# Kernel optimization log

Measured on AMD Instinct MI355X. Metric: run time of the kernel, lower is better.

## Reference

```python
import jax, jax.numpy as jnp
import numpy as np

# Straight-through sign binarization (Binarize in BNN code mutates .data, so
# autograd sees identity -> custom_vjp with identity backward).
@jax.custom_vjp
def binarize(x):
    return jnp.sign(x)

def _bin_fwd(x):
    return jnp.sign(x), None

def _bin_bwd(_, g):
    return (g,)

binarize.defvjp(_bin_fwd, _bin_bwd)

EPS = 1e-5  # torch BatchNorm1d default eps

def batchnorm(x, g, b):
    # training-mode BN: batch statistics, biased variance
    if x.ndim == 3:  # (N, C, L): stats over N and L
        m = x.mean(axis=(0, 2), keepdims=True)
        v = x.var(axis=(0, 2), keepdims=True)
        return (x - m) / jnp.sqrt(v + EPS) * g[None, :, None] + b[None, :, None]
    m = x.mean(axis=0)
    v = x.var(axis=0)
    return (x - m) / jnp.sqrt(v + EPS) * g + b

def hardtanh(x):
    return jnp.clip(x, -1.0, 1.0)

def maxpool3(x):
    # MaxPool1d(kernel=3, stride=3): trim then reshape-max
    N, C, L = x.shape
    Lp = L // 3
    return x[:, :, :Lp * 3].reshape(N, C, Lp, 3).max(axis=-1)

def bconv(x, w, b, binarize_input=True):
    # BinarizeConv1d: kernel 41, dilation 2, VALID padding; weights sign-binarized,
    # inputs binarized except when in_channels == 3 (first layer rule in BNN code).
    xb = binarize(x) if binarize_input else x
    wb = binarize(w)
    y = jax.lax.conv_general_dilated(
        xb, wb, window_strides=(1,), padding='VALID',
        rhs_dilation=(2,), dimension_numbers=('NCH', 'OIH', 'NCH'))
    return y + b[None, :, None]

def blinear(x, w, b):
    # BinarizeLinear: in_features 832/1024 != 784 -> binarize input and weight
    return binarize(x) @ binarize(w).T + b

def _forward(x, bn0_g, bn0_b, conv1_w, conv1_b, bn1_g, bn1_b,
             conv2_w, conv2_b, bn2_g, bn2_b, conv3_w, conv3_b,
             bn3_g, bn3_b, conv4_w, conv4_b, bn4_g, bn4_b,
             conv5_w, conv5_b, fc1_w, fc1_b, bn5_g, bn5_b,
             fc2_w, fc2_b, bn6_g, bn6_b):
    h = hardtanh(batchnorm(x, bn0_g, bn0_b))
    h = maxpool3(bconv(h, conv1_w, conv1_b, binarize_input=False))  # (N,64,5306)
    h = hardtanh(batchnorm(h, bn1_g, bn1_b))
    h = maxpool3(bconv(h, conv2_w, conv2_b))  # (N,64,1742)
    h = hardtanh(batchnorm(h, bn2_g, bn2_b))
    h = maxpool3(bconv(h, conv3_w, conv3_b))  # (N,64,554)
    h = hardtanh(batchnorm(h, bn3_g, bn3_b))
    h = maxpool3(bconv(h, conv4_w, conv4_b))  # (N,64,158)
    h = hardtanh(batchnorm(h, bn4_g, bn4_b))
    h = maxpool3(bconv(h, conv5_w, conv5_b))  # (N,32,26)
    h = h.reshape(-1, 16 * 52)                # (N, 832)
    h = hardtanh(batchnorm(blinear(h, fc1_w, fc1_b), bn5_g, bn5_b))
    h = batchnorm(blinear(h, fc2_w, fc2_b), bn6_g, bn6_b)
    return jax.nn.log_softmax(h, axis=1)

def setup_inputs() -> dict:
    key = jax.random.key(0)
    ks = jax.random.split(key, 32)
    def rn(k, shape, s=0.1):
        return jax.random.normal(k, shape, dtype=jnp.float32) * s
    def bn_params(kg, kb, c):
        return 1.0 + rn(kg, (c,)), rn(kb, (c,))
    N, L, K = 64, 16000, 41
    d = {"x": jax.random.normal(ks[0], (N, 3, L), dtype=jnp.float32)}
    d["bn0_g"], d["bn0_b"] = bn_params(ks[1], ks[2], 3)
    d["conv1_w"], d["conv1_b"] = rn(ks[3], (64, 3, K)), rn(ks[4], (64,), 0.01)
    d["bn1_g"], d["bn1_b"] = bn_params(ks[5], ks[6], 64)
    d["conv2_w"], d["conv2_b"] = rn(ks[7], (64, 64, K)), rn(ks[8], (64,), 0.01)
    d["bn2_g"], d["bn2_b"] = bn_params(ks[9], ks[10], 64)
    d["conv3_w"], d["conv3_b"] = rn(ks[11], (64, 64, K)), rn(ks[12], (64,), 0.01)
    d["bn3_g"], d["bn3_b"] = bn_params(ks[13], ks[14], 64)
    d["conv4_w"], d["conv4_b"] = rn(ks[15], (64, 64, K)), rn(ks[16], (64,), 0.01)
    d["bn4_g"], d["bn4_b"] = bn_params(ks[17], ks[18], 64)
    d["conv5_w"], d["conv5_b"] = rn(ks[19], (32, 64, K)), rn(ks[20], (32,), 0.01)
    d["fc1_w"], d["fc1_b"] = rn(ks[21], (1024, 832)), rn(ks[22], (1024,), 0.01)
    d["bn5_g"], d["bn5_b"] = bn_params(ks[23], ks[24], 1024)
    d["fc2_w"], d["fc2_b"] = rn(ks[25], (1000, 1024)), rn(ks[26], (1000,), 0.01)
    d["bn6_g"], d["bn6_b"] = bn_params(ks[27], ks[28], 1000)
    return d

def reference(x, bn0_g, bn0_b, conv1_w, conv1_b, bn1_g, bn1_b,
              conv2_w, conv2_b, bn2_g, bn2_b, conv3_w, conv3_b,
              bn3_g, bn3_b, conv4_w, conv4_b, bn4_g, bn4_b,
              conv5_w, conv5_b, fc1_w, fc1_b, bn5_g, bn5_b,
              fc2_w, fc2_b, bn6_g, bn6_b):
    return _forward(x, bn0_g, bn0_b, conv1_w, conv1_b, bn1_g, bn1_b,
                    conv2_w, conv2_b, bn2_g, bn2_b, conv3_w, conv3_b,
                    bn3_g, bn3_b, conv4_w, conv4_b, bn4_g, bn4_b,
                    conv5_w, conv5_b, fc1_w, fc1_b, bn5_g, bn5_b,
                    fc2_w, fc2_b, bn6_g, bn6_b)
```

## Files before the change

kernel.cpp:

```cpp
#include <hip/hip_runtime.h>
#include <hip/hip_bf16.h>
#include <stdint.h>

typedef __hip_bfloat16 bf16;
typedef unsigned long long u64;
typedef unsigned short u16;

typedef __attribute__((ext_vector_type(8))) short bf16x8;
typedef __attribute__((ext_vector_type(4))) float f32x4;

#define FIXCAP (1u << 20)

static __device__ __forceinline__ float ldin(const void* p, long i, int f32) {
    return f32 ? ((const float*)p)[i] : __bfloat162float(((const bf16*)p)[i]);
}

__global__ void k_probe(const void* x, unsigned* ctl) {
    int tid = threadIdx.x;
    int good = 0;
    for (int i = tid; i < 1024; i += 256) {
        float v = __bfloat162float(((const bf16*)x)[2 * i]);
        float a = fabsf(v);
        if (v == 0.0f || (isfinite(v) && a >= 1e-4f && a <= 100.0f)) good++;
    }
    __shared__ int s[256];
    s[tid] = good; __syncthreads();
    for (int st = 128; st > 0; st >>= 1) {
        if (tid < st) s[tid] += s[tid + st];
        __syncthreads();
    }
    if (tid == 0) { ctl[0] = 0u; ctl[1] = (s[0] >= 700) ? 0u : 1u; }
}

__global__ void k_sentinel(void* outv, const unsigned* ctl, float val) {
    int i = blockIdx.x * 256 + threadIdx.x;
    if (i >= 64000) return;
    if (ctl[1]) ((float*)outv)[i] = val;
    else ((bf16*)outv)[i] = __float2bfloat16(val);
}

__device__ __forceinline__ void pack_convw_task(const void* w, uint2* wp, int Co, int f32,
                                                int bx, int tid) {
    int t = bx * 256 + tid;
    if (t >= Co * 41) return;
    int co = t / 41, k = t % 41;
    unsigned w0 = 0, w1 = 0;
    for (int c = 0; c < 32; c++)
        if (ldin(w, (co * 64 + c) * 41 + k, f32) > 0.f) w0 |= (1u << c);
    for (int c = 0; c < 32; c++)
        if (ldin(w, (co * 64 + 32 + c) * 41 + k, f32) > 0.f) w1 |= (1u << c);
    wp[t] = make_uint2(w0, w1);
}
__device__ __forceinline__ void pack_rows_task(const void* w, unsigned* wp, int rows, int F,
                                               int f32, int bx, int tid) {
    int Fw = F >> 5;
    int t = bx * 256 + tid;
    if (t >= rows * Fw) return;
    int r = t / Fw, wi = t % Fw;
    unsigned m = 0;
    for (int j = 0; j < 32; j++)
        if (ldin(w, (long)r * F + wi * 32 + j, f32) > 0.f) m |= (1u << j);
    wp[t] = m;
}

__global__ void k_prep(const void* x, const void* c1w, const void* c2w, const void* c3w,
                       const void* c4w, const void* c5w, const void* f1w, const void* f2w,
                       u16* afrag, uint2* w2p, uint2* w3p, uint2* w4p, uint2* w5p,
                       unsigned* fc1wp, unsigned* fc2wp, u64* stats, double* part0,
                       const unsigned* ctl) {
    int f32 = ctl[1];
    int task = blockIdx.y, bx = blockIdx.x, tid = threadIdx.x;
    switch (task) {
        case 0: {
            int t = bx * 256 + tid;
            if (t < 2304) {
                int m = t / 576, rem = t - m * 576;
                int ks = rem / 64, lane = rem - ks * 64;
                int li = lane & 15, hq = lane >> 4;
                int row = 16 * m + li;
                int g = 4 * ks + hq;
                int c = g / 11, t0 = 4 * (g - 11 * c);
                u16* outp = afrag + (size_t)t * 8;
                for (int i2 = 0; i2 < 4; i2++) {
                    int tt = t0 + i2;
                    u16 sv = 0;
                    if (g < 33 && tt <= 40) {
                        float wv = ldin(c1w, (row * 3 + c) * 41 + tt, f32);
                        sv = (wv > 0.f) ? (u16)0x3F80 : ((wv < 0.f) ? (u16)0xBF80 : (u16)0);
                    }
                    outp[2 * i2] = sv;
                    outp[2 * i2 + 1] = sv;
                }
            }
        } break;
        case 1: pack_convw_task(c2w, w2p, 64, f32, bx, tid); break;
        case 2: pack_convw_task(c3w, w3p, 64, f32, bx, tid); break;
        case 3: pack_convw_task(c4w, w4p, 64, f32, bx, tid); break;
        case 4: pack_convw_task(c5w, w5p, 32, f32, bx, tid); break;
        case 5: pack_rows_task(f1w, fc1wp, 1024, 832, f32, bx, tid); break;
        case 6: pack_rows_task(f2w, fc2wp, 1000, 1024, f32, bx, tid); break;
        case 7: {
            int i = bx * 256 + tid;
            if (i < 14400) stats[i] = 0ull;
        } break;
        case 8: {
            if (bx >= 96) return;
            int c = bx >> 5, s = bx & 31;
            double s1 = 0, s2 = 0;
            for (int n = 0; n < 64; n++) {
                long base = (long)(n * 3 + c) * 16000;
                for (int l = s * 256 + tid; l < 16000; l += 32 * 256) {
                    double v = (double)ldin(x, base + l, f32);
                    s1 += v; s2 += v * v;
                }
            }
            __shared__ double a1[256], a2[256];
            a1[tid] = s1; a2[tid] = s2;
            __syncthreads();
            for (int st = 128; st > 0; st >>= 1) {
                if (tid < st) { a1[tid] += a1[tid + st]; a2[tid] += a2[tid + st]; }
                __syncthreads();
            }
            if (tid == 0) { part0[(c * 32 + s) * 2] = a1[0]; part0[(c * 32 + s) * 2 + 1] = a2[0]; }
        } break;
    }
}

__global__ __launch_bounds__(256, 4) void k_conv1(const void* __restrict__ x,
                                                  const double* __restrict__ part0,
                                                  const void* __restrict__ g0,
                                                  const void* __restrict__ b0,
                                                  const u16* __restrict__ afrag,
                                                  float* __restrict__ yq,
                                                  double* __restrict__ yb,
                                                  const unsigned* __restrict__ ctl) {
    __shared__ unsigned xs[8][140];
    __shared__ float pool[4][48][16];
    __shared__ double sbuf[4][64][2];
    __shared__ double2 b0s[3];
    int f32 = ctl[1];
    int n = blockIdx.y, bx = blockIdx.x, tid = threadIdx.x;
    if (tid < 3) {
        int c = tid;
        double s1 = 0, s2 = 0;
        for (int s = 0; s < 32; s++) { s1 += part0[(c * 32 + s) * 2]; s2 += part0[(c * 32 + s) * 2 + 1]; }
        double M = 64.0 * 16000.0;
        double mu = s1 / M, var = s2 / M - mu * mu;
        double A = (double)ldin(g0, c, f32) / sqrt(var + 1e-5);
        b0s[c] = make_double2(A, (double)ldin(b0, c, f32) - mu * A);
    }
    __syncthreads();

    unsigned* xsf = &xs[0][0];
    for (int f = tid; f < 1120; f += 256) {
        int rc = f / 140, qi = f - rc * 140;
        int r = rc >> 2, c = rc & 3;
        unsigned dw = 0u;
        if (c < 3) {
            int xpos = 192 * bx + 2 * qi + r;
            if (xpos < 16000) {
                double2 pb = b0s[c];
                double v = (double)ldin(x, (long)(n * 3 + c) * 16000 + xpos, f32) * pb.x + pb.y;
                v = fmin(fmax(v, -1.0), 1.0);
                float xf = (float)v;
                bf16 h = __float2bfloat16(xf);
                float hf = __bfloat162float(h);
                bf16 lo = __float2bfloat16(xf - hf);
                dw = (unsigned)__bfloat16_as_ushort(h) | ((unsigned)__bfloat16_as_ushort(lo) << 16);
            }
        }
        xsf[f] = dw;
    }
    __syncthreads();

    int lane = tid & 63;
    int li = lane & 15, hq = lane >> 4;
    int w = __builtin_amdgcn_readfirstlane(tid >> 6);

    f32x4 zz = {0.f, 0.f, 0.f, 0.f};
    f32x4 acc[4][3];
#pragma unroll
    for (int m = 0; m < 4; m++)
#pragma unroll
        for (int nf = 0; nf < 3; nf++) acc[m][nf] = zz;

    int boff[3];
#pragma unroll
    for (int nf = 0; nf < 3; nf++) {
        int pl = 48 * w + 16 * nf + li;
        boff[nf] = (pl & 1) * 560 + (pl >> 1);
    }

    const bf16x8* ag = (const bf16x8*)afrag;
#pragma unroll 1
    for (int ks = 0; ks < 9; ks++) {
        int g = 4 * ks + hq;
        int c = g / 11;
        int kb = c * 140 + 4 * (g - 11 * c);
        bf16x8 a0 = ag[(0 * 9 + ks) * 64 + lane];
        bf16x8 a1 = ag[(1 * 9 + ks) * 64 + lane];
        bf16x8 a2 = ag[(2 * 9 + ks) * 64 + lane];
        bf16x8 a3 = ag[(3 * 9 + ks) * 64 + lane];
#pragma unroll
        for (int nf = 0; nf < 3; nf++) {
            const unsigned* bp = xsf + boff[nf] + kb;
            union { int4 i4; bf16x8 v; } u;
            u.i4 = make_int4(bp[0], bp[1], bp[2], bp[3]);
            acc[0][nf] = __builtin_amdgcn_mfma_f32_16x16x32_bf16(a0, u.v, acc[0][nf], 0, 0, 0);
            acc[1][nf] = __builtin_amdgcn_mfma_f32_16x16x32_bf16(a1, u.v, acc[1][nf], 0, 0, 0);
            acc[2][nf] = __builtin_amdgcn_mfma_f32_16x16x32_bf16(a2, u.v, acc[2][nf], 0, 0, 0);
            acc[3][nf] = __builtin_amdgcn_mfma_f32_16x16x32_bf16(a3, u.v, acc[3][nf], 0, 0, 0);
        }
    }

    int lp0 = 64 * bx + 16 * w;
#pragma unroll 1
    for (int m = 0; m < 4; m++) {
#pragma unroll
        for (int nf = 0; nf < 3; nf++)
            *(f32x4*)&pool[w][16 * nf + li][4 * hq] = acc[m][nf];
        double s = 0.0, q = 0.0;
#pragma unroll
        for (int i = 0; i < 4; i++) {
            int pc = hq + 4 * i;
            float mq = fmaxf(fmaxf(pool[w][3 * pc][li], pool[w][3 * pc + 1][li]),
                             pool[w][3 * pc + 2][li]);
            int lp = lp0 + pc;
            if (lp < 5306) {
                yq[((size_t)n * 64 + 16 * m + li) * 5306 + lp] = mq;
                double d = (double)mq;
                s += d; q += d * d;
            }
        }
        s += __shfl_down(s, 32, 64); s += __shfl_down(s, 16, 64);
        q += __shfl_down(q, 32, 64); q += __shfl_down(q, 16, 64);
        if (lane < 16) { sbuf[w][16 * m + lane][0] = s; sbuf[w][16 * m + lane][1] = q; }
    }
    __syncthreads();
    if (tid < 64) {
        double s = sbuf[0][tid][0] + sbuf[1][tid][0] + sbuf[2][tid][0] + sbuf[3][tid][0];
        double q = sbuf[0][tid][1] + sbuf[1][tid][1] + sbuf[2][tid][1] + sbuf[3][tid][1];
        int sb = bx & 15;
        atomicAdd(&yb[(tid * 16 + sb) * 2], s);
        atomicAdd(&yb[(tid * 16 + sb) * 2 + 1], q);
    }
}

__global__ void k_pack_y(const float* __restrict__ yq, const double* __restrict__ yb,
                         const void* g1, const void* b1,
                         uint2* __restrict__ xp,
                         unsigned* __restrict__ fixcnt, unsigned* __restrict__ fixlist,
                         const unsigned* __restrict__ ctl) {
    __shared__ double2 pqs[64];
    int f32 = ctl[1];
    int tid = threadIdx.x;
    if (tid < 64) {
        int c = tid;
        double s1 = 0, s2 = 0;
        for (int s = 0; s < 16; s++) { s1 += yb[(c * 16 + s) * 2]; s2 += yb[(c * 16 + s) * 2 + 1]; }
        double M = 64.0 * 5306.0;
        double mu = s1 / M;
        double var = s2 / M - mu * mu;
        double A = (double)ldin(g1, c, f32) / sqrt(var + 1e-5);
        pqs[c] = make_double2(A, (double)ldin(b1, c, f32) - mu * A);
    }
    __syncthreads();
    int n = blockIdx.y;
    int l = blockIdx.x * 256 + tid;
    if (l >= 5306) return;
    unsigned w0 = 0, w1 = 0;
    for (int c = 0; c < 64; c++) {
        double2 p = pqs[c];
        double v = (double)yq[((size_t)n * 64 + c) * 5306 + l] * p.x + p.y;
        if (fabs(v) < 2e-3 * fabs(p.x)) {
            unsigned idx = atomicAdd(fixcnt, 1u);
            if (idx < FIXCAP) fixlist[idx] = ((unsigned)n << 19) | ((unsigned)c << 13) | (unsigned)l;
        }
        if (v > 0.0) { if (c < 32) w0 |= 1u << c; else w1 |= 1u << (c - 32); }
    }
    xp[(size_t)n * 5306 + l] = make_uint2(w0, w1);
}

__global__ void k_fix(const unsigned* __restrict__ fixcnt, const unsigned* __restrict__ fixlist,
                      const double* __restrict__ yb, const void* g1, const void* b1,
                      const void* __restrict__ x, const void* __restrict__ c1w,
                      const double* __restrict__ part0, const void* g0, const void* b0,
                      unsigned* __restrict__ x2p, const unsigned* __restrict__ ctl) {
    int f32 = ctl[1];
    unsigned cnt = min(*fixcnt, FIXCAP);
    for (unsigned t = blockIdx.x * 256 + threadIdx.x; t < cnt; t += gridDim.x * 256) {
        unsigned e = fixlist[t];
        int n = e >> 19, c = (e >> 13) & 63, l = e & 8191;
        double s1 = 0, s2 = 0;
        for (int s = 0; s < 16; s++) { s1 += yb[(c * 16 + s) * 2]; s2 += yb[(c * 16 + s) * 2 + 1]; }
        double M = 64.0 * 5306.0;
        double mu = s1 / M, var = s2 / M - mu * mu;
        double A = (double)ldin(g1, c, f32) / sqrt(var + 1e-5);
        double B = (double)ldin(b1, c, f32) - mu * A;
        double best = -1e300;
        for (int r = 0; r < 3; r++) {
            int pp = 3 * l + r;
            double acc = 0.0;
            for (int cc = 0; cc < 3; cc++) {
                double p1 = 0, p2 = 0;
                for (int s = 0; s < 32; s++) { p1 += part0[(cc * 32 + s) * 2]; p2 += part0[(cc * 32 + s) * 2 + 1]; }
                double M0 = 64.0 * 16000.0;
                double mu0 = p1 / M0, var0 = p2 / M0 - mu0 * mu0;
                double A0 = (double)ldin(g0, cc, f32) / sqrt(var0 + 1e-5);
                double B0 = (double)ldin(b0, cc, f32) - mu0 * A0;
                for (int k = 0; k < 41; k++) {
                    float wf = ldin(c1w, (c * 3 + cc) * 41 + k, f32);
                    double sgn = (wf > 0.f) ? 1.0 : ((wf < 0.f) ? -1.0 : 0.0);
                    double xv = (double)ldin(x, (long)(n * 3 + cc) * 16000 + pp + 2 * k, f32);
                    xv = fmin(fmax(xv * A0 + B0, -1.0), 1.0);
                    acc = fma(sgn, xv, acc);
                }
            }
            best = fmax(best, acc);
        }
        double v = best * A + B;
        unsigned* word = &x2p[((size_t)n * 5306 + l) * 2 + (c >> 5)];
        unsigned bit = 1u << (c & 31);
        if (v > 0.0) atomicOr(word, bit);
        else atomicAnd(word, ~bit);
    }
}

__global__ __launch_bounds__(256) void k_conv_bin(const uint2* __restrict__ xp,
                                                  const uint2* __restrict__ wp,
                                                  u16* __restrict__ mout,
                                                  int Lp, int Lin, int Co,
                                                  u64* __restrict__ stat) {
    int n = blockIdx.y, tid = threadIdx.x;
    int lane = tid & 63;
    int wave = __builtin_amdgcn_readfirstlane(tid >> 6);
    int co0 = blockIdx.z * 32 + wave * 8;
    int base = blockIdx.x * 192;
    int lp = blockIdx.x * 64 + lane;

    __shared__ uint2 xt[272];
    for (int i = tid; i < 272; i += 256) {
        int pos = base + i;
        xt[i] = (pos < Lin) ? xp[(size_t)n * Lin + pos] : make_uint2(0u, 0u);
    }
    __syncthreads();

    int acc[8][3] = {};
    uint2 xa = xt[3 * lane];
    for (int k = 0; k < 41; k++) {
        uint2 xb = xt[3 * lane + 2 * k + 1];
        uint2 xc = xt[3 * lane + 2 * k + 2];
#pragma unroll
        for (int j = 0; j < 8; j++) {
            uint2 w = wp[(co0 + j) * 41 + k];
            acc[j][0] += __popc(w.x ^ xa.x) + __popc(w.y ^ xa.y);
            acc[j][1] += __popc(w.x ^ xb.x) + __popc(w.y ^ xb.y);
            acc[j][2] += __popc(w.x ^ xc.x) + __popc(w.y ^ xc.y);
        }
        xa = xc;
    }
    bool ok = lp < Lp;
    int sb = blockIdx.x & 15;
#pragma unroll
    for (int j = 0; j < 8; j++) {
        int m = min(min(acc[j][0], acc[j][1]), acc[j][2]);
        if (ok) mout[((size_t)n * Co + co0 + j) * Lp + lp] = (u16)m;
        unsigned s = ok ? (unsigned)m : 0u;
        unsigned q = ok ? (unsigned)(m * m) : 0u;
        for (int off = 32; off > 0; off >>= 1) {
            s += __shfl_down(s, off, 64);
            q += __shfl_down(q, off, 64);
        }
        if (lane == 0) {
            atomicAdd(&stat[((co0 + j) * 16 + sb) * 2], (u64)s);
            atomicAdd(&stat[((co0 + j) * 16 + sb) * 2 + 1], (u64)q);
        }
    }
}

__global__ __launch_bounds__(256) void k_conv_binm(const u16* __restrict__ min_,
                                                   const u64* __restrict__ statIn,
                                                   const void* g, const void* b, double M,
                                                   const uint2* __restrict__ wp,
                                                   u16* __restrict__ mout,
                                                   u64* __restrict__ statOut,
                                                   int Lp, int Lin, int Co,
                                                   const unsigned* __restrict__ ctl) {
    __shared__ double2 pqs[64];
    __shared__ uint2 xt[272];
    int f32 = ctl[1];
    int n = blockIdx.y, tid = threadIdx.x;
    if (tid < 64) {
        int c = tid;
        u64 s1 = 0, s2 = 0;
        for (int s = 0; s < 16; s++) { s1 += statIn[(c * 16 + s) * 2]; s2 += statIn[(c * 16 + s) * 2 + 1]; }
        double mu = (double)s1 / M;
        double varm = (double)s2 / M - mu * mu;
        double A = (double)ldin(g, c, f32) / sqrt(4.0 * varm + 1e-5);
        pqs[c] = make_double2(-2.0 * A, 2.0 * A * mu + (double)ldin(b, c, f32));
    }
    __syncthreads();
    int base = blockIdx.x * 192;
    for (int i = tid; i < 272; i += 256) {
        int pos = base + i;
        unsigned w0 = 0, w1 = 0;
        if (pos < Lin) {
            const u16* mp = min_ + (size_t)n * 64 * Lin + pos;
#pragma unroll 4
            for (int c = 0; c < 32; c++) {
                double2 p = pqs[c];
                if ((double)mp[(size_t)c * Lin] * p.x + p.y > 0.0) w0 |= 1u << c;
            }
#pragma unroll 4
            for (int c = 0; c < 32; c++) {
                double2 p = pqs[c + 32];
                if ((double)mp[(size_t)(c + 32) * Lin] * p.x + p.y > 0.0) w1 |= 1u << c;
            }
        }
        xt[i] = make_uint2(w0, w1);
    }
    __syncthreads();

    int lane = tid & 63;
    int wave = __builtin_amdgcn_readfirstlane(tid >> 6);
    int co0 = blockIdx.z * 32 + wave * 8;
    int lp = blockIdx.x * 64 + lane;

    int acc[8][3] = {};
    uint2 xa = xt[3 * lane];
    for (int k = 0; k < 41; k++) {
        uint2 xb = xt[3 * lane + 2 * k + 1];
        uint2 xc = xt[3 * lane + 2 * k + 2];
#pragma unroll
        for (int j = 0; j < 8; j++) {
            uint2 w = wp[(co0 + j) * 41 + k];
            acc[j][0] += __popc(w.x ^ xa.x) + __popc(w.y ^ xa.y);
            acc[j][1] += __popc(w.x ^ xb.x) + __popc(w.y ^ xb.y);
            acc[j][2] += __popc(w.x ^ xc.x) + __popc(w.y ^ xc.y);
        }
        xa = xc;
    }
    bool ok = lp < Lp;
    int sb = blockIdx.x & 15;
#pragma unroll
    for (int j = 0; j < 8; j++) {
        int m = min(min(acc[j][0], acc[j][1]), acc[j][2]);
        if (ok) mout[((size_t)n * Co + co0 + j) * Lp + lp] = (u16)m;
        if (statOut) {
            unsigned s = ok ? (unsigned)m : 0u;
            unsigned q = ok ? (unsigned)(m * m) : 0u;
            for (int off = 32; off > 0; off >>= 1) {
                s += __shfl_down(s, off, 64);
                q += __shfl_down(q, off, 64);
            }
            if (lane == 0) {
                atomicAdd(&statOut[((co0 + j) * 16 + sb) * 2], (u64)s);
                atomicAdd(&statOut[((co0 + j) * 16 + sb) * 2 + 1], (u64)q);
            }
        }
    }
}

__global__ void k_c5fc1(const u16* __restrict__ m4, const u64* __restrict__ s4,
                        const void* g4, const void* b4,
                        const uint2* __restrict__ w5p, const void* __restrict__ b5,
                        const unsigned* __restrict__ fc1wp, u16* __restrict__ acc1,
                        u64* __restrict__ s5, const unsigned* __restrict__ ctl) {
    __shared__ double2 pqs[64];
    __shared__ uint2 xt[280];
    __shared__ int m5s[32][26];
    __shared__ unsigned xw[26];
    int f32 = ctl[1];
    int n = blockIdx.x, tid = threadIdx.x;
    const int Lin = 158;
    if (tid < 64) {
        int c = tid;
        u64 s1 = 0, s2 = 0;
        for (int s = 0; s < 16; s++) { s1 += s4[(c * 16 + s) * 2]; s2 += s4[(c * 16 + s) * 2 + 1]; }
        double M = 64.0 * 158.0;
        double mu = (double)s1 / M;
        double varm = (double)s2 / M - mu * mu;
        double A = (double)ldin(g4, c, f32) / sqrt(4.0 * varm + 1e-5);
        pqs[c] = make_double2(-2.0 * A, 2.0 * A * mu + (double)ldin(b4, c, f32));
    }
    __syncthreads();
    for (int i = tid; i < 280; i += 256) {
        unsigned w0 = 0, w1 = 0;
        if (i < Lin) {
            const u16* mp = m4 + (size_t)n * 64 * Lin + i;
#pragma unroll 4
            for (int c = 0; c < 32; c++) {
                double2 p = pqs[c];
                if ((double)mp[(size_t)c * Lin] * p.x + p.y > 0.0) w0 |= 1u << c;
            }
#pragma unroll 4
            for (int c = 0; c < 32; c++) {
                double2 p = pqs[c + 32];
                if ((double)mp[(size_t)(c + 32) * Lin] * p.x + p.y > 0.0) w1 |= 1u << c;
            }
        }
        xt[i] = make_uint2(w0, w1);
    }
    __syncthreads();

    int lane = tid & 63;
    int wave = __builtin_amdgcn_readfirstlane(tid >> 6);
    int co0 = wave * 8;
    int acc[8][3] = {};
    uint2 xa = xt[3 * lane];
    for (int k = 0; k < 41; k++) {
        uint2 xb = xt[3 * lane + 2 * k + 1];
        uint2 xc = xt[3 * lane + 2 * k + 2];
#pragma unroll
        for (int j = 0; j < 8; j++) {
            uint2 w = w5p[(co0 + j) * 41 + k];
            acc[j][0] += __popc(w.x ^ xa.x) + __popc(w.y ^ xa.y);
            acc[j][1] += __popc(w.x ^ xb.x) + __popc(w.y ^ xb.y);
            acc[j][2] += __popc(w.x ^ xc.x) + __popc(w.y ^ xc.y);
        }
        xa = xc;
    }
    if (lane < 26) {
#pragma unroll
        for (int j = 0; j < 8; j++)
            m5s[co0 + j][lane] = min(min(acc[j][0], acc[j][1]), acc[j][2]);
    }
    __syncthreads();
    if (tid < 26) {
        unsigned mask = 0;
        for (int j = 0; j < 32; j++) {
            int f = tid * 32 + j, c = f / 26, l = f % 26;
            double yv = 2624.0 - 2.0 * (double)m5s[c][l] + (double)ldin(b5, c, f32);
            if (yv > 0.0) mask |= 1u << j;
        }
        xw[tid] = mask;
    }
    __syncthreads();
#pragma unroll
    for (int i = 0; i < 4; i++) {
        int j = tid + i * 256;
        unsigned a = 0;
        for (int w = 0; w < 26; w++) a += __popc(xw[w] ^ fc1wp[j * 26 + w]);
        acc1[n * 1024 + j] = (u16)a;
        atomicAdd(&s5[j * 2], (u64)a);
        atomicAdd(&s5[j * 2 + 1], (u64)(a * a));
    }
}

__global__ void k_fc2(const u16* __restrict__ acc1, const u64* __restrict__ s5,
                      const void* g5, const void* b5, const unsigned* __restrict__ fc2wp,
                      u16* __restrict__ acc2, u64* __restrict__ s6, const unsigned* ctl) {
    __shared__ double2 pq5s[1024];
    __shared__ unsigned xw[32];
    int f32 = ctl[1];
    int n = blockIdx.y, tid = threadIdx.x;
    for (int f = tid; f < 1024; f += 256) {
        u64 a1 = s5[f * 2], a2 = s5[f * 2 + 1];
        double mu = (double)a1 / 64.0;
        double varm = (double)a2 / 64.0 - mu * mu;
        double A = (double)ldin(g5, f, f32) / sqrt(4.0 * varm + 1e-5);
        pq5s[f] = make_double2(-2.0 * A, 2.0 * A * mu + (double)ldin(b5, f, f32));
    }
    __syncthreads();
    if (tid < 32) {
        unsigned mask = 0;
        for (int j = 0; j < 32; j++) {
            int f = tid * 32 + j;
            double2 p = pq5s[f];
            if ((double)acc1[n * 1024 + f] * p.x + p.y > 0.0) mask |= 1u << j;
        }
        xw[tid] = mask;
    }
    __syncthreads();
    int j = blockIdx.x * 256 + tid;
    if (j >= 1000) return;
    unsigned a = 0;
    for (int w = 0; w < 32; w++) a += __popc(xw[w] ^ fc2wp[j * 32 + w]);
    acc2[n * 1000 + j] = (u16)a;
    atomicAdd(&s6[j * 2], (u64)a);
    atomicAdd(&s6[j * 2 + 1], (u64)(a * a));
}

__global__ void k_lsm(const u16* __restrict__ acc2, const u64* __restrict__ s6,
                      const void* g6, const void* b6, const unsigned* ctl, void* outv) {
    int n = blockIdx.x, tid = threadIdx.x;
    int f32 = ctl[1];
    __shared__ double red[256];
    double v[4];
    double mx = -1e300;
#pragma unroll
    for (int i = 0; i < 4; i++) {
        int j = tid + i * 256;
        if (j < 1000) {
            u64 a1 = s6[j * 2], a2 = s6[j * 2 + 1];
            double mu = (double)a1 / 64.0;
            double varm = (double)a2 / 64.0 - mu * mu;
            double A = (double)ldin(g6, j, f32) / sqrt(4.0 * varm + 1e-5);
            v[i] = (double)acc2[n * 1000 + j] * (-2.0 * A) + (2.0 * A * mu + (double)ldin(b6, j, f32));
            mx = fmax(mx, v[i]);
        } else v[i] = -1e300;
    }
    red[tid] = mx; __syncthreads();
    for (int s = 128; s > 0; s >>= 1) {
        if (tid < s) red[tid] = fmax(red[tid], red[tid + s]);
        __syncthreads();
    }
    mx = red[0]; __syncthreads();
    double sum = 0.0;
#pragma unroll
    for (int i = 0; i < 4; i++) {
        int j = tid + i * 256;
        if (j < 1000) sum += exp(v[i] - mx);
    }
    red[tid] = sum; __syncthreads();
    for (int s = 128; s > 0; s >>= 1) {
        if (tid < s) red[tid] += red[tid + s];
        __syncthreads();
    }
    double ls = log(red[0]);
#pragma unroll
    for (int i = 0; i < 4; i++) {
        int j = tid + i * 256;
        if (j < 1000) {
            float r = (float)(v[i] - mx - ls);
            if (!isfinite(r)) r = -700.0f;
            if (f32) ((float*)outv)[n * 1000 + j] = r;
            else ((bf16*)outv)[n * 1000 + j] = __float2bfloat16(r);
        }
    }
}

extern "C" void kernel_launch(void* const* d_in, const int* in_sizes, int n_in,
                              void* d_out, int out_size, void* d_ws, size_t ws_size,
                              hipStream_t stream) {
    const void* x       = d_in[0];
    const void* bn0_g   = d_in[1];
    const void* bn0_b   = d_in[2];
    const void* conv1_w = d_in[3];
    const void* bn1_g   = d_in[5];
    const void* bn1_b   = d_in[6];
    const void* conv2_w = d_in[7];
    const void* bn2_g   = d_in[9];
    const void* bn2_b   = d_in[10];
    const void* conv3_w = d_in[11];
    const void* bn3_g   = d_in[13];
    const void* bn3_b   = d_in[14];
    const void* conv4_w = d_in[15];
    const void* bn4_g   = d_in[17];
    const void* bn4_b   = d_in[18];
    const void* conv5_w = d_in[19];
    const void* conv5_b = d_in[20];
    const void* fc1_w   = d_in[21];
    const void* bn5_g   = d_in[23];
    const void* bn5_b   = d_in[24];
    const void* fc2_w   = d_in[25];
    const void* bn6_g   = d_in[27];
    const void* bn6_b   = d_in[28];

    char* wsb = (char*)d_ws;
    size_t off = 0;
    auto alloc = [&](size_t bytes) -> void* {
        off = (off + 255) & ~(size_t)255;
        void* p = wsb + off;
        off += bytes;
        return p;
    };

    unsigned* ctl   = (unsigned*)alloc(256);
    unsigned* x2p   = (unsigned*)alloc(2716672);
    float*    yq    = (float*)alloc(86933504);
    u16*      m2    = (u16*)alloc(14270464);
    u16*      m3    = (u16*)alloc(4538368);
    u16*      m4    = (u16*)alloc(1294336);
    u16*      acc1  = (u16*)alloc(131072);
    u16*      acc2  = (u16*)alloc(128000);
    u16*      afrag = (u16*)alloc(36864);
    uint2*    w2p   = (uint2*)alloc(20992);
    uint2*    w3p   = (uint2*)alloc(20992);
    uint2*    w4p   = (uint2*)alloc(20992);
    uint2*    w5p   = (uint2*)alloc(10496);
    unsigned* fc1wp = (unsigned*)alloc(106496);
    unsigned* fc2wp = (unsigned*)alloc(128000);
    u64*      stats = (u64*)alloc(14400 * 8);
    double*   part0 = (double*)alloc(2048);
    unsigned* fixlist = (unsigned*)alloc(FIXCAP * 4);
    size_t need = (off + 255) & ~(size_t)255;

    u64* s2 = stats;
    u64* s3 = stats + 2048;
    u64* s4 = stats + 4096;
    u64* s5 = stats + 6144;
    u64* s6 = stats + 8192;
    double* yb = (double*)(stats + 12288);
    unsigned* fixcnt = (unsigned*)(stats + 14340);

    k_probe<<<1, 256, 0, stream>>>(x, ctl);

    if (n_in != 29) {
        k_sentinel<<<250, 256, 0, stream>>>(d_out, ctl, -(3000.0f + (float)n_in));
        return;
    }
    if (ws_size < need) {
        k_sentinel<<<250, 256, 0, stream>>>(d_out, ctl, -1500.0f);
        return;
    }

    k_prep<<<dim3(125, 9), 256, 0, stream>>>(x, conv1_w, conv2_w, conv3_w, conv4_w, conv5_w,
                                             fc1_w, fc2_w, afrag, w2p, w3p, w4p, w5p,
                                             fc1wp, fc2wp, stats, part0, ctl);

    k_conv1<<<dim3(83, 64), 256, 0, stream>>>(x, part0, bn0_g, bn0_b, afrag, yq, yb, ctl);
    k_pack_y<<<dim3(21, 64), 256, 0, stream>>>(yq, yb, bn1_g, bn1_b, (uint2*)x2p,
                                               fixcnt, fixlist, ctl);
    k_fix<<<64, 256, 0, stream>>>(fixcnt, fixlist, yb, bn1_g, bn1_b, x, conv1_w,
                                  part0, bn0_g, bn0_b, x2p, ctl);

    k_conv_bin<<<dim3(28, 64, 2), 256, 0, stream>>>((const uint2*)x2p, w2p, m2, 1742, 5306, 64, s2);
    k_conv_binm<<<dim3(9, 64, 2), 256, 0, stream>>>(m2, s2, bn2_g, bn2_b, 64.0 * 1742.0,
                                                    w3p, m3, s3, 554, 1742, 64, ctl);
    k_conv_binm<<<dim3(3, 64, 2), 256, 0, stream>>>(m3, s3, bn3_g, bn3_b, 64.0 * 554.0,
                                                    w4p, m4, s4, 158, 554, 64, ctl);

    k_c5fc1<<<64, 256, 0, stream>>>(m4, s4, bn4_g, bn4_b, w5p, conv5_b, fc1wp, acc1, s5, ctl);
    k_fc2<<<dim3(4, 64), 256, 0, stream>>>(acc1, s5, bn5_g, bn5_b, fc2wp, acc2, s6, ctl);
    k_lsm<<<64, 256, 0, stream>>>(acc2, s6, bn6_g, bn6_b, ctl, d_out);
}
```

Before: 795.9 us.

## Recompute conv1 in a second pass instead of storing fp32 pooled output

The first conv1 launch now only accumulates batch-norm statistics. A second conv1 launch recomputes the MFMA convolution and max-pool, applies BN1, and packs sign bits directly into the bitplane buffer, which replaces k_pack_y. This removes the ~87 MB fp32 intermediate write and its re-read in exchange for running the convolution twice. The BN0 input transform also moves from double to float, which slightly changes input rounding before the split-bf16 encoding.

Measured after the change: 806.4 us. Within noise of the previous version (+1.3%).

```diff
diff --git a/kernel.cpp b/kernel.cpp
--- a/kernel.cpp
+++ b/kernel.cpp
@@ -131,13 +131,20 @@
                                                   const void* __restrict__ g0,
                                                   const void* __restrict__ b0,
                                                   const u16* __restrict__ afrag,
-                                                  float* __restrict__ yq,
                                                   double* __restrict__ yb,
-                                                  const unsigned* __restrict__ ctl) {
+                                                  const void* __restrict__ g1,
+                                                  const void* __restrict__ b1,
+                                                  uint2* __restrict__ x2p,
+                                                  unsigned* __restrict__ fixcnt,
+                                                  unsigned* __restrict__ fixlist,
+                                                  const unsigned* __restrict__ ctl,
+                                                  int pass) {
     __shared__ unsigned xs[8][140];
-    __shared__ float pool[4][48][16];
+    __shared__ float pool[4][48][20];
     __shared__ double sbuf[4][64][2];
-    __shared__ double2 b0s[3];
+    __shared__ unsigned char sb[4][16][64];
+    __shared__ double2 pqs[64];
+    __shared__ float2 b0f[3];
     int f32 = ctl[1];
     int n = blockIdx.y, bx = blockIdx.x, tid = threadIdx.x;
     if (tid < 3) {
@@ -147,7 +154,16 @@
         double M = 64.0 * 16000.0;
         double mu = s1 / M, var = s2 / M - mu * mu;
         double A = (double)ldin(g0, c, f32) / sqrt(var + 1e-5);
-        b0s[c] = make_double2(A, (double)ldin(b0, c, f32) - mu * A);
+        b0f[c] = make_float2((float)A, (float)((double)ldin(b0, c, f32) - mu * A));
+    }
+    if (pass && tid >= 64 && tid < 128) {
+        int c = tid - 64;
+        double s1 = 0, s2 = 0;
+        for (int s = 0; s < 16; s++) { s1 += yb[(c * 16 + s) * 2]; s2 += yb[(c * 16 + s) * 2 + 1]; }
+        double M = 64.0 * 5306.0;
+        double mu = s1 / M, var = s2 / M - mu * mu;
+        double A = (double)ldin(g1, c, f32) / sqrt(var + 1e-5);
+        pqs[c] = make_double2(A, (double)ldin(b1, c, f32) - mu * A);
     }
     __syncthreads();
 
@@ -159,13 +175,12 @@
         if (c < 3) {
             int xpos = 192 * bx + 2 * qi + r;
             if (xpos < 16000) {
-                double2 pb = b0s[c];
-                double v = (double)ldin(x, (long)(n * 3 + c) * 16000 + xpos, f32) * pb.x + pb.y;
-                v = fmin(fmax(v, -1.0), 1.0);
-                float xf = (float)v;
-                bf16 h = __float2bfloat16(xf);
+                float2 pb = b0f[c];
+                float v = fmaf(ldin(x, (long)(n * 3 + c) * 16000 + xpos, f32), pb.x, pb.y);
+                v = fminf(fmaxf(v, -1.f), 1.f);
+                bf16 h = __float2bfloat16(v);
                 float hf = __bfloat162float(h);
-                bf16 lo = __float2bfloat16(xf - hf);
+                bf16 lo = __float2bfloat16(v - hf);
                 dw = (unsigned)__bfloat16_as_ushort(h) | ((unsigned)__bfloat16_as_ushort(lo) << 16);
             }
         }
@@ -214,71 +229,77 @@
     }
 
     int lp0 = 64 * bx + 16 * w;
+    if (pass == 0) {
 #pragma unroll 1
-    for (int m = 0; m < 4; m++) {
-#pragma unroll
-        for (int nf = 0; nf < 3; nf++)
-            *(f32x4*)&pool[w][16 * nf + li][4 * hq] = acc[m][nf];
-        double s = 0.0, q = 0.0;
-#pragma unroll
-        for (int i = 0; i < 4; i++) {
-            int pc = hq + 4 * i;
-            float mq = fmaxf(fmaxf(pool[w][3 * pc][li], pool[w][3 * pc + 1][li]),
-                             pool[w][3 * pc + 2][li]);
-            int lp = lp0 + pc;
+        for (int m = 0; m < 4; m++) {
+#pragma unroll
+            for (int nf = 0; nf < 3; nf++)
+                *(f32x4*)&pool[w][16 * nf + li][4 * hq] = acc[m][nf];
+            double s = 0.0, q = 0.0;
+#pragma unroll
+            for (int i = 0; i < 4; i++) {
+                int pc = hq + 4 * i;
+                float mq = fmaxf(fmaxf(pool[w][3 * pc][li], pool[w][3 * pc + 1][li]),
+                                 pool[w][3 * pc + 2][li]);
+                if (lp0 + pc < 5306) {
+                    double d = (double)mq;
+                    s += d; q += d * d;
+                }
+            }
+            s += __shfl_down(s, 32, 64); s += __shfl_down(s, 16, 64);
+            q += __shfl_down(q, 32, 64); q += __shfl_down(q, 16, 64);
+            if (lane < 16) { sbuf[w][16 * m + lane][0] = s; sbuf[w][16 * m + lane][1] = q; }
+        }
+        __syncthreads();
+        if (tid < 64) {
+            double s = sbuf[0][tid][0] + sbuf[1][tid][0] + sbuf[2][tid][0] + sbuf[3][tid][0];
+            double q = sbuf[0][tid][1] + sbuf[1][tid][1] + sbuf[2][tid][1] + sbuf[3][tid][1];
+            int sbk = bx & 15;
+            atomicAdd(&yb[(tid * 16 + sbk) * 2], s);
+            atomicAdd(&yb[(tid * 16 + sbk) * 2 + 1], q);
+        }
+    } else {
+#pragma unroll 1
+        for (int m = 0; m < 4; m++) {
+#pragma unroll
+            for (int nf = 0; nf < 3; nf++)
+                *(f32x4*)&pool[w][16 * nf + li][4 * hq] = acc[m][nf];
+            int c = 16 * m + li;
+            double2 P = pqs[c];
+            double athr = 2e-3 * fabs(P.x);
+#pragma unroll
+            for (int i = 0; i < 4; i++) {
+                int pc = hq + 4 * i;
+                int lp = lp0 + pc;
+                float mq = fmaxf(fmaxf(pool[w][3 * pc][li], pool[w][3 * pc + 1][li]),
+                                 pool[w][3 * pc + 2][li]);
+                if (lp < 5306) {
+                    double v = (double)mq * P.x + P.y;
+                    sb[w][pc][c] = (v > 0.0) ? 1 : 0;
+                    if (fabs(v) < athr) {
+                        unsigned idx = atomicAdd(fixcnt, 1u);
+                        if (idx < FIXCAP)
+                            fixlist[idx] = ((unsigned)n << 19) | ((unsigned)c << 13) | (unsigned)lp;
+                    }
+                }
+            }
+        }
+        __syncthreads();
+        if (tid < 64) {
+            int lp = 64 * bx + tid;
             if (lp < 5306) {
-                yq[((size_t)n * 64 + 16 * m + li) * 5306 + lp] = mq;
-                double d = (double)mq;
-                s += d; q += d * d;
-            }
-        }
-        s += __shfl_down(s, 32, 64); s += __shfl_down(s, 16, 64);
-        q += __shfl_down(q, 32, 64); q += __shfl_down(q, 16, 64);
-        if (lane < 16) { sbuf[w][16 * m + lane][0] = s; sbuf[w][16 * m + lane][1] = q; }
-    }
-    __syncthreads();
-    if (tid < 64) {
-        double s = sbuf[0][tid][0] + sbuf[1][tid][0] + sbuf[2][tid][0] + sbuf[3][tid][0];
-        double q = sbuf[0][tid][1] + sbuf[1][tid][1] + sbuf[2][tid][1] + sbuf[3][tid][1];
-        int sb = bx & 15;
-        atomicAdd(&yb[(tid * 16 + sb) * 2], s);
-        atomicAdd(&yb[(tid * 16 + sb) * 2 + 1], q);
-    }
-}
-
-__global__ void k_pack_y(const float* __restrict__ yq, const double* __restrict__ yb,
-                         const void* g1, const void* b1,
-                         uint2* __restrict__ xp,
-                         unsigned* __restrict__ fixcnt, unsigned* __restrict__ fixlist,
-                         const unsigned* __restrict__ ctl) {
-    __shared__ double2 pqs[64];
-    int f32 = ctl[1];
-    int tid = threadIdx.x;
-    if (tid < 64) {
-        int c = tid;
-        double s1 = 0, s2 = 0;
-        for (int s = 0; s < 16; s++) { s1 += yb[(c * 16 + s) * 2]; s2 += yb[(c * 16 + s) * 2 + 1]; }
-        double M = 64.0 * 5306.0;
-        double mu = s1 / M;
-        double var = s2 / M - mu * mu;
-        double A = (double)ldin(g1, c, f32) / sqrt(var + 1e-5);
-        pqs[c] = make_double2(A, (double)ldin(b1, c, f32) - mu * A);
-    }
-    __syncthreads();
-    int n = blockIdx.y;
-    int l = blockIdx.x * 256 + tid;
-    if (l >= 5306) return;
-    unsigned w0 = 0, w1 = 0;
-    for (int c = 0; c < 64; c++) {
-        double2 p = pqs[c];
-        double v = (double)yq[((size_t)n * 64 + c) * 5306 + l] * p.x + p.y;
-        if (fabs(v) < 2e-3 * fabs(p.x)) {
-            unsigned idx = atomicAdd(fixcnt, 1u);
-            if (idx < FIXCAP) fixlist[idx] = ((unsigned)n << 19) | ((unsigned)c << 13) | (unsigned)l;
-        }
-        if (v > 0.0) { if (c < 32) w0 |= 1u << c; else w1 |= 1u << (c - 32); }
-    }
-    xp[(size_t)n * 5306 + l] = make_uint2(w0, w1);
+                const unsigned* sp = (const unsigned*)&sb[tid >> 4][tid & 15][0];
+                unsigned w0 = 0, w1 = 0;
+#pragma unroll
+                for (int jw = 0; jw < 8; jw++)
+                    w0 |= (((sp[jw] * 0x01020408u) >> 24) & 0xFu) << (4 * jw);
+#pragma unroll
+                for (int jw = 8; jw < 16; jw++)
+                    w1 |= (((sp[jw] * 0x01020408u) >> 24) & 0xFu) << (4 * (jw - 8));
+                x2p[(size_t)n * 5306 + lp] = make_uint2(w0, w1);
+            }
+        }
+    }
 }
 
 __global__ void k_fix(const unsigned* __restrict__ fixcnt, const unsigned* __restrict__ fixlist,
@@ -668,7 +689,6 @@
 
     unsigned* ctl   = (unsigned*)alloc(256);
     unsigned* x2p   = (unsigned*)alloc(2716672);
-    float*    yq    = (float*)alloc(86933504);
     u16*      m2    = (u16*)alloc(14270464);
     u16*      m3    = (u16*)alloc(4538368);
     u16*      m4    = (u16*)alloc(1294336);
@@ -709,9 +729,12 @@
                                              fc1_w, fc2_w, afrag, w2p, w3p, w4p, w5p,
                                              fc1wp, fc2wp, stats, part0, ctl);
 
-    k_conv1<<<dim3(83, 64), 256, 0, stream>>>(x, part0, bn0_g, bn0_b, afrag, yq, yb, ctl);
-    k_pack_y<<<dim3(21, 64), 256, 0, stream>>>(yq, yb, bn1_g, bn1_b, (uint2*)x2p,
-                                               fixcnt, fixlist, ctl);
+    k_conv1<<<dim3(83, 64), 256, 0, stream>>>(x, part0, bn0_g, bn0_b, afrag, yb,
+                                              bn1_g, bn1_b, (uint2*)x2p,
+                                              fixcnt, fixlist, ctl, 0);
+    k_conv1<<<dim3(83, 64), 256, 0, stream>>>(x, part0, bn0_g, bn0_b, afrag, yb,
+                                              bn1_g, bn1_b, (uint2*)x2p,
+                                              fixcnt, fixlist, ctl, 1);
     k_fix<<<64, 256, 0, stream>>>(fixcnt, fixlist, yb, bn1_g, bn1_b, x, conv1_w,
                                   part0, bn0_g, bn0_b, x2p, ctl);
 
```
